# Optimization experiments

Measured on AMD Instinct MI355X. Metric: run time of the kernel, lower is better.

Reference implementation:

```python
import jax, jax.numpy as jnp
import numpy as np

WINDOW_SIZE = 11
N_CHANNELS = 3
SIGMA = 1.5
K1, K2 = 0.01, 0.03
VALUE_RANGE = 1.0


def _create_window(window_size: int, n_channels: int, sigma: float) -> np.ndarray:
    # 1D gaussian, normalized, then outer product -> 2D kernel
    coords = np.arange(window_size, dtype=np.float32) - (window_size - 1) / 2.0
    g = np.exp(-(coords ** 2) / (2.0 * sigma ** 2))
    g = g / g.sum()
    k2d = np.outer(g, g).astype(np.float32)  # (K, K), sums to 1
    # depthwise kernel, OIHW with I=1 (groups = n_channels)
    return np.broadcast_to(k2d, (n_channels, 1, window_size, window_size)).copy()


def _dwconv(x, window):
    # depthwise valid conv, NCHW / OIHW
    return jax.lax.conv_general_dilated(
        x, window, window_strides=(1, 1), padding='VALID',
        feature_group_count=window.shape[0],
        dimension_numbers=('NCHW', 'OIHW', 'NCHW'))


def setup_inputs() -> dict:
    key = jax.random.key(0)
    kx, ky = jax.random.split(key)
    N, C, H, W = 32, N_CHANNELS, 512, 512
    x = jax.random.uniform(kx, (N, C, H, W), dtype=jnp.float32)
    y = jax.random.uniform(ky, (N, C, H, W), dtype=jnp.float32)
    window = jnp.asarray(_create_window(WINDOW_SIZE, N_CHANNELS, SIGMA))
    return {"x": x, "y": y, "window": window}


def reference(x, y, window):
    c1 = (K1 * VALUE_RANGE) ** 2
    c2 = (K2 * VALUE_RANGE) ** 2

    mu_x = _dwconv(x, window)
    mu_y = _dwconv(y, window)
    mu_x_sq = mu_x ** 2
    mu_y_sq = mu_y ** 2
    mu_xy = mu_x * mu_y

    sigma_x_sq = _dwconv(x * x, window) - mu_x_sq
    sigma_y_sq = _dwconv(y * y, window) - mu_y_sq
    sigma_xy = _dwconv(x * y, window) - mu_xy

    cs = (2.0 * sigma_xy + c2) / (sigma_x_sq + sigma_y_sq + c2)
    ss = (2.0 * mu_xy + c1) / (mu_x_sq + mu_y_sq + c1) * cs

    l = ss.mean(axis=(-1, -2))  # (N, C) per-channel SSIM
    l = l.mean(axis=-1)         # (N,)  per-sample
    return l.mean()             # reduction='mean'
```

## Files before the change

kernel.cpp:

```cpp
#include <hip/hip_runtime.h>

#define KS    11
#define HH    512
#define WW    512
#define OUTD  502
#define OH    34
#define ROWS  44
#define NB    15
#define NIMG  96
#define PADW  524

__global__ __launch_bounds__(256, 2)
void ssim_main(const float* __restrict__ xg, const float* __restrict__ yg,
               const float* __restrict__ win, double* __restrict__ acc_out)
{
    __shared__ float xs[2][PADW];
    __shared__ float ys[2][PADW];
    __shared__ float wsums[4];

    const int tid  = threadIdx.x;
    const int img  = blockIdx.x % NIMG;
    const int band = blockIdx.x / NIMG;
    const int row0 = band * OH;
    const int c0   = 2 * tid;

    float g[KS];
    #pragma unroll
    for (int i = 0; i < KS; i++) {
        float s = 0.f;
        #pragma unroll
        for (int j = 0; j < KS; j++) s += win[i * KS + j];
        g[i] = s;
    }

    if (tid < (PADW - WW)) {
        xs[0][WW + tid] = 0.f; xs[1][WW + tid] = 0.f;
        ys[0][WW + tid] = 0.f; ys[1][WW + tid] = 0.f;
    }

    const float* xi = xg + (size_t)img * HH * WW;
    const float* yi = yg + (size_t)img * HH * WW;

    float acc[5][2][KS];
    #pragma unroll
    for (int q = 0; q < 5; q++)
        #pragma unroll
        for (int c = 0; c < 2; c++)
            #pragma unroll
            for (int s = 0; s < KS; s++) acc[q][c][s] = 0.f;

    float ssum = 0.f;

    const float C1 = 0.0001f;
    const float C2 = 0.0009f;

    float2 vx, vy;
    {
        int gr = row0; if (gr > HH - 1) gr = HH - 1;
        vx = *(const float2*)&xi[(size_t)gr * WW + c0];
        vy = *(const float2*)&yi[(size_t)gr * WW + c0];
        xs[0][c0] = vx.x; xs[0][c0 + 1] = vx.y;
        ys[0][c0] = vy.x; ys[0][c0 + 1] = vy.y;
        gr = row0 + 1; if (gr > HH - 1) gr = HH - 1;
        vx = *(const float2*)&xi[(size_t)gr * WW + c0];
        vy = *(const float2*)&yi[(size_t)gr * WW + c0];
    }
    __syncthreads();

    #pragma unroll 1
    for (int rb = 0; rb < ROWS / KS; rb++) {
        #pragma unroll
        for (int rr = 0; rr < KS; rr++) {
            const int r = rb * KS + rr;

            const float* xb = xs[r & 1];
            const float* yb = ys[r & 1];
            float xv[12], yv[12];
            #pragma unroll
            for (int k = 0; k < 6; k++) {
                float2 a = *(const float2*)&xb[c0 + 2 * k];
                float2 b = *(const float2*)&yb[c0 + 2 * k];
                xv[2 * k] = a.x; xv[2 * k + 1] = a.y;
                yv[2 * k] = b.x; yv[2 * k + 1] = b.y;
            }

            if (r + 1 < ROWS) {
                float* xw = xs[(r + 1) & 1];
                float* yw = ys[(r + 1) & 1];
                xw[c0] = vx.x; xw[c0 + 1] = vx.y;
                yw[c0] = vy.x; yw[c0 + 1] = vy.y;
            }
            if (r + 2 < ROWS) {
                int gr = row0 + r + 2; if (gr > HH - 1) gr = HH - 1;
                vx = *(const float2*)&xi[(size_t)gr * WW + c0];
                vy = *(const float2*)&yi[(size_t)gr * WW + c0];
            }

            float xx[12], yy[12], xy[12];
            #pragma unroll
            for (int k = 0; k < 12; k++) {
                xx[k] = xv[k] * xv[k];
                yy[k] = yv[k] * yv[k];
                xy[k] = xv[k] * yv[k];
            }

            float h[5][2];
            #pragma unroll
            for (int q = 0; q < 5; q++) { h[q][0] = 0.f; h[q][1] = 0.f; }
            #pragma unroll
            for (int j = 0; j < KS; j++) {
                const float gj = g[j];
                h[0][0] = fmaf(gj, xv[j], h[0][0]); h[0][1] = fmaf(gj, xv[j + 1], h[0][1]);
                h[1][0] = fmaf(gj, yv[j], h[1][0]); h[1][1] = fmaf(gj, yv[j + 1], h[1][1]);
                h[2][0] = fmaf(gj, xx[j], h[2][0]); h[2][1] = fmaf(gj, xx[j + 1], h[2][1]);
                h[3][0] = fmaf(gj, yy[j], h[3][0]); h[3][1] = fmaf(gj, yy[j + 1], h[3][1]);
                h[4][0] = fmaf(gj, xy[j], h[4][0]); h[4][1] = fmaf(gj, xy[j + 1], h[4][1]);
            }

            #pragma unroll
            for (int i = 0; i < KS; i++) {
                const int slot = (rr - i + KS) % KS;
                const float gi = g[i];
                #pragma unroll
                for (int q = 0; q < 5; q++) {
                    acc[q][0][slot] = fmaf(gi, h[q][0], acc[q][0][slot]);
                    acc[q][1][slot] = fmaf(gi, h[q][1], acc[q][1][slot]);
                }
            }

            const int es   = (rr + 1) % KS;
            const int jloc = r - (KS - 1);
            if (jloc >= 0 && (row0 + jloc) < OUTD) {
                #pragma unroll
                for (int c = 0; c < 2; c++) {
                    if (c0 + c < OUTD) {
                        const float mx  = acc[0][c][es], my  = acc[1][c][es];
                        const float Sxx = acc[2][c][es], Syy = acc[3][c][es], Sxy = acc[4][c][es];
                        const float mxx = mx * mx, myy = my * my, mxy = mx * my;
                        const float sxx = Sxx - mxx, syy = Syy - myy, sxy = Sxy - mxy;
                        const float num = (2.f * mxy + C1) * (2.f * sxy + C2);
                        const float den = (mxx + myy + C1) * (sxx + syy + C2);
                        float rc = __builtin_amdgcn_rcpf(den);
                        rc = rc * fmaf(-den, rc, 2.0f);
                        ssum = fmaf(num, rc, ssum);
                    }
                }
            }
            #pragma unroll
            for (int q = 0; q < 5; q++) { acc[q][0][es] = 0.f; acc[q][1][es] = 0.f; }

            __syncthreads();
        }
    }

    #pragma unroll
    for (int off = 32; off > 0; off >>= 1)
        ssum += __shfl_down(ssum, off);
    const int wave = tid >> 6;
    if ((tid & 63) == 0) wsums[wave] = ssum;
    __syncthreads();
    if (tid == 0) {
        float s = wsums[0] + wsums[1] + wsums[2] + wsums[3];
        atomicAdd(acc_out, (double)s);
    }
}

__global__ void ssim_finalize(const double* __restrict__ acc, float* __restrict__ out)
{
    out[0] = (float)(acc[0] * (1.0 / 24192384.0));
}

extern "C" void kernel_launch(void* const* d_in, const int* in_sizes, int n_in,
                              void* d_out, int out_size, void* d_ws, size_t ws_size,
                              hipStream_t stream)
{
    const float* x   = (const float*)d_in[0];
    const float* y   = (const float*)d_in[1];
    const float* win = (const float*)d_in[2];
    float* out = (float*)d_out;
    double* acc = (double*)d_ws;

    hipMemsetAsync(acc, 0, sizeof(double), stream);
    ssim_main<<<dim3(NIMG * NB), dim3(256), 0, stream>>>(x, y, win, acc);
    ssim_finalize<<<dim3(1), dim3(1), 0, stream>>>(acc, out);
}
```

Baseline: 280.6 us.

## Use sum/difference signals to cut SSIM moments from five to four

The kernel now stages s=x+y and d=x-y in shared memory instead of x and y. It convolves only s, d, s² and d², then recovers the SSIM terms algebraically. This drops one of five accumulator sets and the cross-product work, which frees registers. Bands are also made taller (8 bands of 67 output rows) and launch bounds raised to 3 blocks per SIMD, to cut halo re-reads and fit the grid in fewer waves. The trade-off is more cancellation in float differences such as Ss-Sd and a-b, and less parallel slack with fewer blocks.

```diff
diff --git a/kernel.cpp b/kernel.cpp
--- a/kernel.cpp
+++ b/kernel.cpp
@@ -4,18 +4,18 @@
 #define HH    512
 #define WW    512
 #define OUTD  502
-#define OH    34
-#define ROWS  44
-#define NB    15
+#define OH    67
+#define ROWS  77
+#define NB    8
 #define NIMG  96
 #define PADW  524
 
-__global__ __launch_bounds__(256, 2)
+__global__ __launch_bounds__(256, 3)
 void ssim_main(const float* __restrict__ xg, const float* __restrict__ yg,
                const float* __restrict__ win, double* __restrict__ acc_out)
 {
-    __shared__ float xs[2][PADW];
-    __shared__ float ys[2][PADW];
+    __shared__ float shs[2][PADW];
+    __shared__ float shd[2][PADW];
     __shared__ float wsums[4];
 
     const int tid  = threadIdx.x;
@@ -34,16 +34,16 @@
     }
 
     if (tid < (PADW - WW)) {
-        xs[0][WW + tid] = 0.f; xs[1][WW + tid] = 0.f;
-        ys[0][WW + tid] = 0.f; ys[1][WW + tid] = 0.f;
+        shs[0][WW + tid] = 0.f; shs[1][WW + tid] = 0.f;
+        shd[0][WW + tid] = 0.f; shd[1][WW + tid] = 0.f;
     }
 
     const float* xi = xg + (size_t)img * HH * WW;
     const float* yi = yg + (size_t)img * HH * WW;
 
-    float acc[5][2][KS];
+    float acc[4][2][KS];
     #pragma unroll
-    for (int q = 0; q < 5; q++)
+    for (int q = 0; q < 4; q++)
         #pragma unroll
         for (int c = 0; c < 2; c++)
             #pragma unroll
@@ -51,19 +51,21 @@
 
     float ssum = 0.f;
 
-    const float C1 = 0.0001f;
-    const float C2 = 0.0009f;
+    const float C1x2 = 0.0002f;
+    const float C2x2 = 0.0018f;
 
-    float2 vx, vy;
+    float2 pfs, pfd;
     {
         int gr = row0; if (gr > HH - 1) gr = HH - 1;
-        vx = *(const float2*)&xi[(size_t)gr * WW + c0];
-        vy = *(const float2*)&yi[(size_t)gr * WW + c0];
-        xs[0][c0] = vx.x; xs[0][c0 + 1] = vx.y;
-        ys[0][c0] = vy.x; ys[0][c0 + 1] = vy.y;
+        float2 ax = *(const float2*)&xi[(size_t)gr * WW + c0];
+        float2 ay = *(const float2*)&yi[(size_t)gr * WW + c0];
+        shs[0][c0] = ax.x + ay.x; shs[0][c0 + 1] = ax.y + ay.y;
+        shd[0][c0] = ax.x - ay.x; shd[0][c0 + 1] = ax.y - ay.y;
         gr = row0 + 1; if (gr > HH - 1) gr = HH - 1;
-        vx = *(const float2*)&xi[(size_t)gr * WW + c0];
-        vy = *(const float2*)&yi[(size_t)gr * WW + c0];
+        ax = *(const float2*)&xi[(size_t)gr * WW + c0];
+        ay = *(const float2*)&yi[(size_t)gr * WW + c0];
+        pfs = make_float2(ax.x + ay.x, ax.y + ay.y);
+        pfd = make_float2(ax.x - ay.x, ax.y - ay.y);
     }
     __syncthreads();
 
@@ -73,59 +75,59 @@
         for (int rr = 0; rr < KS; rr++) {
             const int r = rb * KS + rr;
 
-            const float* xb = xs[r & 1];
-            const float* yb = ys[r & 1];
-            float xv[12], yv[12];
+            const float* sb = shs[r & 1];
+            const float* db = shd[r & 1];
+            float sv[12], dv[12];
             #pragma unroll
             for (int k = 0; k < 6; k++) {
-                float2 a = *(const float2*)&xb[c0 + 2 * k];
-                float2 b = *(const float2*)&yb[c0 + 2 * k];
-                xv[2 * k] = a.x; xv[2 * k + 1] = a.y;
-                yv[2 * k] = b.x; yv[2 * k + 1] = b.y;
+                float2 a = *(const float2*)&sb[c0 + 2 * k];
+                float2 b = *(const float2*)&db[c0 + 2 * k];
+                sv[2 * k] = a.x; sv[2 * k + 1] = a.y;
+                dv[2 * k] = b.x; dv[2 * k + 1] = b.y;
             }
 
             if (r + 1 < ROWS) {
-                float* xw = xs[(r + 1) & 1];
-                float* yw = ys[(r + 1) & 1];
-                xw[c0] = vx.x; xw[c0 + 1] = vx.y;
-                yw[c0] = vy.x; yw[c0 + 1] = vy.y;
+                float* sw = shs[(r + 1) & 1];
+                float* dw = shd[(r + 1) & 1];
+                sw[c0] = pfs.x; sw[c0 + 1] = pfs.y;
+                dw[c0] = pfd.x; dw[c0 + 1] = pfd.y;
             }
             if (r + 2 < ROWS) {
                 int gr = row0 + r + 2; if (gr > HH - 1) gr = HH - 1;
-                vx = *(const float2*)&xi[(size_t)gr * WW + c0];
-                vy = *(const float2*)&yi[(size_t)gr * WW + c0];
+                float2 ax = *(const float2*)&xi[(size_t)gr * WW + c0];
+                float2 ay = *(const float2*)&yi[(size_t)gr * WW + c0];
+                pfs = make_float2(ax.x + ay.x, ax.y + ay.y);
+                pfd = make_float2(ax.x - ay.x, ax.y - ay.y);
             }
 
-            float xx[12], yy[12], xy[12];
-            #pragma unroll
-            for (int k = 0; k < 12; k++) {
-                xx[k] = xv[k] * xv[k];
-                yy[k] = yv[k] * yv[k];
-                xy[k] = xv[k] * yv[k];
-            }
-
-            float h[5][2];
-            #pragma unroll
-            for (int q = 0; q < 5; q++) { h[q][0] = 0.f; h[q][1] = 0.f; }
+            float h0a = 0.f, h0b = 0.f, h1a = 0.f, h1b = 0.f;
+            float h2a = 0.f, h2b = 0.f, h3a = 0.f, h3b = 0.f;
+            float ts = sv[0] * sv[0];
+            float td = dv[0] * dv[0];
             #pragma unroll
             for (int j = 0; j < KS; j++) {
-                const float gj = g[j];
-                h[0][0] = fmaf(gj, xv[j], h[0][0]); h[0][1] = fmaf(gj, xv[j + 1], h[0][1]);
-                h[1][0] = fmaf(gj, yv[j], h[1][0]); h[1][1] = fmaf(gj, yv[j + 1], h[1][1]);
-                h[2][0] = fmaf(gj, xx[j], h[2][0]); h[2][1] = fmaf(gj, xx[j + 1], h[2][1]);
-                h[3][0] = fmaf(gj, yy[j], h[3][0]); h[3][1] = fmaf(gj, yy[j + 1], h[3][1]);
-                h[4][0] = fmaf(gj, xy[j], h[4][0]); h[4][1] = fmaf(gj, xy[j + 1], h[4][1]);
+                const float gj  = g[j];
+                const float tsn = sv[j + 1] * sv[j + 1];
+                const float tdn = dv[j + 1] * dv[j + 1];
+                h0a = fmaf(gj, sv[j],     h0a); h0b = fmaf(gj, sv[j + 1], h0b);
+                h1a = fmaf(gj, dv[j],     h1a); h1b = fmaf(gj, dv[j + 1], h1b);
+                h2a = fmaf(gj, ts,        h2a); h2b = fmaf(gj, tsn,       h2b);
+                h3a = fmaf(gj, td,        h3a); h3b = fmaf(gj, tdn,       h3b);
+                ts = tsn; td = tdn;
             }
 
             #pragma unroll
             for (int i = 0; i < KS; i++) {
                 const int slot = (rr - i + KS) % KS;
                 const float gi = g[i];
-                #pragma unroll
-                for (int q = 0; q < 5; q++) {
-                    acc[q][0][slot] = fmaf(gi, h[q][0], acc[q][0][slot]);
-                    acc[q][1][slot] = fmaf(gi, h[q][1], acc[q][1][slot]);
-                }
+                acc[0][0][slot] = fmaf(gi, h0a, acc[0][0][slot]);
+                acc[0][1][slot] = fmaf(gi, h0b, acc[0][1][slot]);
+                acc[1][0][slot] = fmaf(gi, h1a, acc[1][0][slot]);
+                acc[1][1][slot] = fmaf(gi, h1b, acc[1][1][slot]);
+                acc[2][0][slot] = fmaf(gi, h2a, acc[2][0][slot]);
+                acc[2][1][slot] = fmaf(gi, h2b, acc[2][1][slot]);
+                acc[3][0][slot] = fmaf(gi, h3a, acc[3][0][slot]);
+                acc[3][1][slot] = fmaf(gi, h3b, acc[3][1][slot]);
             }
 
             const int es   = (rr + 1) % KS;
@@ -134,12 +136,15 @@
                 #pragma unroll
                 for (int c = 0; c < 2; c++) {
                     if (c0 + c < OUTD) {
-                        const float mx  = acc[0][c][es], my  = acc[1][c][es];
-                        const float Sxx = acc[2][c][es], Syy = acc[3][c][es], Sxy = acc[4][c][es];
-                        const float mxx = mx * mx, myy = my * my, mxy = mx * my;
-                        const float sxx = Sxx - mxx, syy = Syy - myy, sxy = Sxy - mxy;
-                        const float num = (2.f * mxy + C1) * (2.f * sxy + C2);
-                        const float den = (mxx + myy + C1) * (sxx + syy + C2);
+                        const float ms = acc[0][c][es], md = acc[1][c][es];
+                        const float Ss = acc[2][c][es], Sd = acc[3][c][es];
+                        const float a = ms * ms, b = md * md;
+                        const float P = a - b;
+                        const float Q = a + b;
+                        const float U = Ss - Sd;
+                        const float V = Ss + Sd;
+                        const float num = (P + C1x2) * ((U - P) + C2x2);
+                        const float den = (Q + C1x2) * ((V - Q) + C2x2);
                         float rc = __builtin_amdgcn_rcpf(den);
                         rc = rc * fmaf(-den, rc, 2.0f);
                         ssum = fmaf(num, rc, ssum);
@@ -147,7 +152,7 @@
                 }
             }
             #pragma unroll
-            for (int q = 0; q < 5; q++) { acc[q][0][es] = 0.f; acc[q][1][es] = 0.f; }
+            for (int q = 0; q < 4; q++) { acc[q][0][es] = 0.f; acc[q][1][es] = 0.f; }
 
             __syncthreads();
         }
```

Result: slower. 402.9 us (+43.6%).
